# Optimization experiments

Hardware: AMD Instinct MI355X
Metric: run time of the kernel (lower is better)

The kernel has to match this reference:

```python
import jax, jax.numpy as jnp
import numpy as np

N_NODES = 100000

def setup_inputs() -> dict:
    key = jax.random.key(0)
    k1, k2, k3 = jax.random.split(key, 3)
    x = jax.random.normal(k1, (N_NODES, 64), dtype=jnp.float32)
    edge_index = jax.random.randint(k2, (2, 1250000), 0, N_NODES, dtype=jnp.int64)
    edge_weight = jax.random.uniform(k3, (1250000,), dtype=jnp.float32)
    return {"x": x, "edge_index": edge_index, "edge_weight": edge_weight}

def reference(x, edge_index, edge_weight):
    # LightGCNConv: out[dst] = sum_e edge_weight[e] * x[src_e]  (aggr='add')
    src, dst = edge_index[0], edge_index[1]
    msgs = edge_weight[:, None] * x[src]          # [E, d] gather-multiply
    out = jax.ops.segment_sum(msgs, dst, num_segments=N_NODES)  # scatter-add
    return out
```

## Files before the change

### kernel.cpp

```cpp
#include <hip/hip_runtime.h>
#include <hip/hip_bf16.h>


#define N_NODES   100000
#define N_FEAT    64

#define A_BSH     7
#define A_NPB     (1 << A_BSH)
#define A_KB      ((N_NODES + A_NPB - 1) >> A_BSH)
#define A_CAP     2048
#define A_FCHUNK  4096
#define A_OVCAP   65536
#define NBIN      ((1250000 + A_FCHUNK - 1) / A_FCHUNK)
#define NCAST     391

__global__ __launch_bounds__(1024) void k_castbin(
    const float* __restrict__ x, ushort* __restrict__ xb,
    const int* __restrict__ ei, const float* __restrict__ w,
    int* __restrict__ bcur, int2* __restrict__ stg,
    int* __restrict__ ovf, int* __restrict__ ovcnt, int E) {
    int t = threadIdx.x;
    if (blockIdx.x >= NBIN) {
        int cb = blockIdx.x - NBIN;
        #pragma unroll
        for (int k = 0; k < 4; ++k) {
            int i4 = cb * 4096 + k * 1024 + t;
            if (i4 < N_NODES * N_FEAT / 4) {
                float4 v = ((const float4*)x)[i4];
                uint4 u = *(uint4*)&v;
                ushort4 r;
                r.x = (ushort)((u.x + 0x7FFFu + ((u.x >> 16) & 1)) >> 16);
                r.y = (ushort)((u.y + 0x7FFFu + ((u.y >> 16) & 1)) >> 16);
                r.z = (ushort)((u.z + 0x7FFFu + ((u.z >> 16) & 1)) >> 16);
                r.w = (ushort)((u.w + 0x7FFFu + ((u.w >> 16) & 1)) >> 16);
                ((ushort4*)xb)[i4] = r;
            }
        }
        return;
    }
    __shared__ int h[A_KB];
    for (int b = t; b < A_KB; b += 1024) h[b] = 0;
    __syncthreads();
    int e0 = blockIdx.x * A_FCHUNK;
    int dstv[A_FCHUNK / 1024];
    int srcv[A_FCHUNK / 1024];
    float wv[A_FCHUNK / 1024];
    #pragma unroll
    for (int k = 0; k < A_FCHUNK / 1024; ++k) {
        int e = e0 + k * 1024 + t;
        bool ok = (e < E);
        dstv[k] = ok ? ei[E + e] : -1;
        srcv[k] = ok ? ei[e] : 0;
        wv[k]   = ok ? w[e] : 0.f;
        if (ok) atomicAdd(&h[dstv[k] >> A_BSH], 1);
    }
    __syncthreads();
    for (int b = t; b < A_KB; b += 1024) {
        int c = h[b];
        h[b] = c ? atomicAdd(&bcur[b], c) : 0;
    }
    __syncthreads();
    #pragma unroll
    for (int k = 0; k < A_FCHUNK / 1024; ++k) {
        if (dstv[k] >= 0) {
            int b = dstv[k] >> A_BSH;
            int loc = atomicAdd(&h[b], 1);
            if (loc < A_CAP) {
                stg[b * A_CAP + loc] =
                    make_int2(srcv[k] | ((dstv[k] & (A_NPB - 1)) << 17),
                              __float_as_int(wv[k]));
            } else {
                int oi = atomicAdd(ovcnt, 1);
                if (oi < A_OVCAP) ovf[oi] = e0 + k * 1024 + t;
            }
        }
    }
}

__global__ __launch_bounds__(1024) void k_sortgather(
    const ushort* __restrict__ xb, const int* __restrict__ bcur,
    const int2* __restrict__ stg, float* __restrict__ out) {
    __shared__ int2 buf[A_CAP];
    __shared__ int2 srt[A_CAP];
    __shared__ int  hist[A_NPB];
    __shared__ int  start[A_NPB];
    __shared__ int  cur[A_NPB];
    int b = blockIdx.x, t = threadIdx.x;
    int cnt = bcur[b];
    if (cnt > A_CAP) cnt = A_CAP;
    int base = b * A_CAP;

    if (t < A_NPB) hist[t] = 0;
    __syncthreads();
    for (int i = t; i < cnt; i += 1024) {
        int2 p = stg[base + i];
        buf[i] = p;
        atomicAdd(&hist[(p.x >> 17) & (A_NPB - 1)], 1);
    }
    __syncthreads();
    if (t < A_NPB) cur[t] = hist[t];
    __syncthreads();
    for (int off = 1; off < A_NPB; off <<= 1) {
        int v = (t < A_NPB && t >= off) ? cur[t - off] : 0;
        __syncthreads();
        if (t < A_NPB && t >= off) cur[t] += v;
        __syncthreads();
    }
    if (t < A_NPB) start[t] = (t == 0) ? 0 : cur[t - 1];
    __syncthreads();
    if (t < A_NPB) cur[t] = start[t];
    __syncthreads();
    for (int i = t; i < cnt; i += 1024) {
        int2 p = buf[i];
        int pos = atomicAdd(&cur[(p.x >> 17) & (A_NPB - 1)], 1);
        srt[pos] = p;
    }
    __syncthreads();

    int wid  = t >> 6;
    int lane = t & 63;
    int q    = lane >> 4;
    int l    = lane & 15;
    const ushort4* xb4 = (const ushort4*)xb;
    #pragma unroll
    for (int pass = 0; pass < 2; ++pass) {
        int n = pass * 64 + wid * 4 + q;
        int node = (b << A_BSH) + n;
        int j = start[n], end = start[n] + hist[n];
        float ax0 = 0.f, ay0 = 0.f, az0 = 0.f, aw0 = 0.f;
        float ax1 = 0.f, ay1 = 0.f, az1 = 0.f, aw1 = 0.f;
        for (; j + 1 < end; j += 2) {
            int2 p0 = srt[j];
            int2 p1 = srt[j + 1];
            ushort4 u0 = xb4[(size_t)(p0.x & 0x1FFFF) * 16 + l];
            ushort4 u1 = xb4[(size_t)(p1.x & 0x1FFFF) * 16 + l];
            float w0 = __int_as_float(p0.y), w1 = __int_as_float(p1.y);
            ax0 += w0 * __uint_as_float((uint)u0.x << 16);
            ay0 += w0 * __uint_as_float((uint)u0.y << 16);
            az0 += w0 * __uint_as_float((uint)u0.z << 16);
            aw0 += w0 * __uint_as_float((uint)u0.w << 16);
            ax1 += w1 * __uint_as_float((uint)u1.x << 16);
            ay1 += w1 * __uint_as_float((uint)u1.y << 16);
            az1 += w1 * __uint_as_float((uint)u1.z << 16);
            aw1 += w1 * __uint_as_float((uint)u1.w << 16);
        }
        if (j < end) {
            int2 p = srt[j];
            ushort4 u = xb4[(size_t)(p.x & 0x1FFFF) * 16 + l];
            float wv = __int_as_float(p.y);
            ax0 += wv * __uint_as_float((uint)u.x << 16);
            ay0 += wv * __uint_as_float((uint)u.y << 16);
            az0 += wv * __uint_as_float((uint)u.z << 16);
            aw0 += wv * __uint_as_float((uint)u.w << 16);
        }
        if (node < N_NODES) {
            float4 r;
            r.x = ax0 + ax1; r.y = ay0 + ay1;
            r.z = az0 + az1; r.w = aw0 + aw1;
            ((float4*)out)[(size_t)node * 16 + l] = r;
        }
    }
}

__global__ __launch_bounds__(256) void k_ovf(
    const float* __restrict__ x, const int* __restrict__ ei,
    const float* __restrict__ w, const int* __restrict__ ovf,
    const int* __restrict__ ovcnt, float* __restrict__ out, int E) {
    int n = *ovcnt;
    if (n > A_OVCAP) n = A_OVCAP;
    int wid  = blockIdx.x * 4 + (threadIdx.x >> 6);
    int lane = threadIdx.x & 63;
    for (int i = wid; i < n; i += gridDim.x * 4) {
        int e = ovf[i];
        float v = w[e] * x[(size_t)ei[e] * N_FEAT + lane];
        atomicAdd(&out[(size_t)ei[E + e] * N_FEAT + lane], v);
    }
}

#define BSH       8
#define NPB       (1 << BSH)
#define KB        ((N_NODES + NPB - 1) >> BSH)
#define FCHUNK    8192
#define SORT_CAP  4096

__global__ __launch_bounds__(256) void k_chist(
    const int* __restrict__ ei, int* __restrict__ bcur, int E) {
    __shared__ int h[KB];
    int t = threadIdx.x;
    for (int b = t; b < KB; b += 256) h[b] = 0;
    __syncthreads();
    int e0 = blockIdx.x * FCHUNK;
    #pragma unroll
    for (int k = 0; k < FCHUNK / 256; ++k) {
        int e = e0 + k * 256 + t;
        if (e < E) atomicAdd(&h[ei[E + e] >> BSH], 1);
    }
    __syncthreads();
    for (int b = t; b < KB; b += 256) if (h[b]) atomicAdd(&bcur[b], h[b]);
}

__global__ __launch_bounds__(256) void k_cscan(
    int* __restrict__ bcur, int* __restrict__ boffs) {
    __shared__ int sdata[256];
    int t = threadIdx.x;
    int i0 = 2 * t, i1 = 2 * t + 1;
    int v0 = (i0 < KB) ? bcur[i0] : 0;
    int v1 = (i1 < KB) ? bcur[i1] : 0;
    sdata[t] = v0 + v1; __syncthreads();
    for (int off = 1; off < 256; off <<= 1) {
        int v = (t >= off) ? sdata[t - off] : 0;
        __syncthreads();
        if (t >= off) sdata[t] += v;
        __syncthreads();
    }
    int run = (t == 0) ? 0 : sdata[t - 1];
    if (i0 < KB) { boffs[i0] = run; bcur[i0] = run; }
    run += v0;
    if (i1 < KB) { boffs[i1] = run; bcur[i1] = run; }
    if (t == 255) boffs[KB] = sdata[255];
}

__global__ __launch_bounds__(256) void k_cbin(
    const int* __restrict__ ei, const float* __restrict__ w,
    int* __restrict__ bcur, int2* __restrict__ stg, int E) {
    __shared__ int h[KB];
    int t = threadIdx.x;
    for (int b = t; b < KB; b += 256) h[b] = 0;
    __syncthreads();
    int e0 = blockIdx.x * FCHUNK;
    #pragma unroll
    for (int k = 0; k < FCHUNK / 256; ++k) {
        int e = e0 + k * 256 + t;
        if (e < E) atomicAdd(&h[ei[E + e] >> BSH], 1);
    }
    __syncthreads();
    for (int b = t; b < KB; b += 256) {
        int c = h[b];
        h[b] = c ? atomicAdd(&bcur[b], c) : 0;
    }
    __syncthreads();
    #pragma unroll
    for (int k = 0; k < FCHUNK / 256; ++k) {
        int e = e0 + k * 256 + t;
        if (e < E) {
            int dst = ei[E + e];
            int slot = atomicAdd(&h[dst >> BSH], 1);
            stg[slot] = make_int2(ei[e] | ((dst & (NPB - 1)) << 17),
                                  __float_as_int(w[e]));
        }
    }
}

__global__ __launch_bounds__(256) void k_csort(
    int2* __restrict__ stg, const int* __restrict__ boffs,
    int* __restrict__ offs) {
    __shared__ int2 buf[SORT_CAP];
    __shared__ int  hist[NPB];
    __shared__ int  cur[NPB];
    __shared__ int  sdata[256];
    int b = blockIdx.x, t = threadIdx.x;
    int bg = boffs[b], end = boffs[b + 1], cnt = end - bg;
    for (int n = t; n < NPB; n += 256) hist[n] = 0;
    __syncthreads();
    int nlds = cnt < SORT_CAP ? cnt : SORT_CAP;
    for (int i = t; i < nlds; i += 256) {
        int2 p = stg[bg + i];
        buf[i] = p;
        atomicAdd(&hist[(p.x >> 17) & (NPB - 1)], 1);
    }
    int2 r0{0,0}, r1{0,0}; int nr = 0;
    {
        int i0 = nlds + t, i1 = nlds + 256 + t;
        if (i0 < cnt) { r0 = stg[bg + i0]; atomicAdd(&hist[(r0.x >> 17) & (NPB - 1)], 1); nr = 1; }
        if (i1 < cnt) { r1 = stg[bg + i1]; atomicAdd(&hist[(r1.x >> 17) & (NPB - 1)], 1); nr = 2; }
    }
    __syncthreads();
    int c = hist[t];
    sdata[t] = c; __syncthreads();
    for (int off = 1; off < 256; off <<= 1) {
        int v = (t >= off) ? sdata[t - off] : 0;
        __syncthreads();
        if (t >= off) sdata[t] += v;
        __syncthreads();
    }
    int excl = (t == 0) ? 0 : sdata[t - 1];
    cur[t] = excl;
    int node = (b << BSH) + t;
    if (node < N_NODES) offs[node] = bg + excl;
    if (b == KB - 1 && t == 255) offs[N_NODES] = end;
    __syncthreads();
    for (int i = t; i < nlds; i += 256) {
        int2 p = buf[i];
        int pos = atomicAdd(&cur[(p.x >> 17) & (NPB - 1)], 1);
        stg[bg + pos] = p;
    }
    if (nr >= 1) { int pos = atomicAdd(&cur[(r0.x >> 17) & (NPB - 1)], 1); stg[bg + pos] = r0; }
    if (nr >= 2) { int pos = atomicAdd(&cur[(r1.x >> 17) & (NPB - 1)], 1); stg[bg + pos] = r1; }
}

__global__ __launch_bounds__(256) void k_gather(
    const float* __restrict__ x, const int* __restrict__ offs,
    const int2* __restrict__ stg, float* __restrict__ out) {
    int node = blockIdx.x * 4 + (threadIdx.x >> 6);
    int lane = threadIdx.x & 63;
    if (node >= N_NODES) return;
    int bg = offs[node], end = offs[node + 1];
    float a0 = 0.f, a1 = 0.f, a2 = 0.f, a3 = 0.f;
    int j = bg;
    for (; j + 3 < end; j += 4) {
        int2 p0 = stg[j];
        int2 p1 = stg[j + 1];
        int2 p2 = stg[j + 2];
        int2 p3 = stg[j + 3];
        a0 += __int_as_float(p0.y) * x[(size_t)(p0.x & 0x1FFFF) * N_FEAT + lane];
        a1 += __int_as_float(p1.y) * x[(size_t)(p1.x & 0x1FFFF) * N_FEAT + lane];
        a2 += __int_as_float(p2.y) * x[(size_t)(p2.x & 0x1FFFF) * N_FEAT + lane];
        a3 += __int_as_float(p3.y) * x[(size_t)(p3.x & 0x1FFFF) * N_FEAT + lane];
    }
    for (; j < end; ++j) {
        int2 p = stg[j];
        a0 += __int_as_float(p.y) * x[(size_t)(p.x & 0x1FFFF) * N_FEAT + lane];
    }
    out[(size_t)node * N_FEAT + lane] = (a0 + a1) + (a2 + a3);
}

__global__ __launch_bounds__(256) void gnn_scatter_kernel(
    const float* __restrict__ x, const int* __restrict__ ei,
    const float* __restrict__ w, float* __restrict__ out, int E) {
    int e = blockIdx.x * 4 + (threadIdx.x >> 6);
    int lane = threadIdx.x & 63;
    if (e >= E) return;
    float v = w[e] * x[(size_t)ei[e] * N_FEAT + lane];
    atomicAdd(&out[(size_t)ei[E + e] * N_FEAT + lane], v);
}

static inline size_t align16(size_t v) { return (v + 15) & ~(size_t)15; }

extern "C" void kernel_launch(void* const* d_in, const int* in_sizes, int n_in,
                              void* d_out, int out_size, void* d_ws, size_t ws_size,
                              hipStream_t stream) {
    const float* x   = (const float*)d_in[0];
    const int*   ei  = (const int*)d_in[1];
    const float* w   = (const float*)d_in[2];
    float*       out = (float*)d_out;
    const int E = in_sizes[2];
    char* ws = (char*)d_ws;

    size_t a_xb   = 0;
    size_t a_stg  = align16(a_xb + (size_t)N_NODES * N_FEAT * 2);
    size_t a_bcur = align16(a_stg + (size_t)A_KB * A_CAP * 8);
    size_t a_ovf  = align16(a_bcur + (size_t)(A_KB + 1) * 4);
    size_t need_a = a_ovf + (size_t)A_OVCAP * 4;

    if (ws_size >= need_a && E == 1250000) {
        ushort* xb    = (ushort*)(ws + a_xb);
        int2*   stg   = (int2*)(ws + a_stg);
        int*    bcur  = (int*)(ws + a_bcur);
        int*    ovcnt = bcur + A_KB;
        int*    ovf   = (int*)(ws + a_ovf);

        hipMemsetAsync(bcur, 0, (size_t)(A_KB + 1) * 4, stream);
        k_castbin<<<NBIN + NCAST, 1024, 0, stream>>>(
            x, xb, ei, w, bcur, stg, ovf, ovcnt, E);
        k_sortgather<<<A_KB, 1024, 0, stream>>>(xb, bcur, stg, out);
        k_ovf<<<16, 256, 0, stream>>>(x, ei, w, ovf, ovcnt, out, E);
        return;
    }

    size_t b_bcur  = 0;
    size_t b_boffs = align16(b_bcur + (size_t)KB * 4);
    size_t b_offs  = align16(b_boffs + (size_t)(KB + 1) * 4);
    size_t b_stg   = align16(b_offs + (size_t)(N_NODES + 1) * 4);
    size_t need_b  = b_stg + (size_t)E * 8;

    if (ws_size >= need_b) {
        int*  bcur  = (int*)(ws + b_bcur);
        int*  boffs = (int*)(ws + b_boffs);
        int*  offs  = (int*)(ws + b_offs);
        int2* stg   = (int2*)(ws + b_stg);
        const int nblk = (E + FCHUNK - 1) / FCHUNK;
        hipMemsetAsync(bcur, 0, (size_t)KB * 4, stream);
        k_chist<<<nblk, 256, 0, stream>>>(ei, bcur, E);
        k_cscan<<<1, 256, 0, stream>>>(bcur, boffs);
        k_cbin<<<nblk, 256, 0, stream>>>(ei, w, bcur, stg, E);
        k_csort<<<KB, 256, 0, stream>>>(stg, boffs, offs);
        k_gather<<<(N_NODES + 3) / 4, 256, 0, stream>>>(x, offs, stg, out);
        return;
    }

    hipMemsetAsync(d_out, 0, (size_t)out_size * sizeof(float), stream);
    gnn_scatter_kernel<<<(E + 3) / 4, 256, 0, stream>>>(x, ei, w, out, E);
}
```

Baseline: 135.6 us.

## Vectorize edge loads, degree-sort nodes, and gather with 8 lanes per node

The binning kernel now loads each thread's four consecutive edges with int4/float4 vector loads instead of four strided scalar loads. In the gather kernel, nodes are bitonic-sorted by in-degree within each bucket so that wavefronts process nodes of similar degree, which is meant to reduce divergence from uneven loop lengths. Each node now uses 8 lanes with 16-byte bf16 loads instead of 16 lanes with 8-byte loads, so all 128 nodes are handled in one pass. The cost is an extra shared-memory sort with many __syncthreads barriers, and more registers per thread for the wider accumulators.

```diff
diff --git a/kernel.cpp b/kernel.cpp
--- a/kernel.cpp
+++ b/kernel.cpp
@@ -42,18 +42,28 @@
     for (int b = t; b < A_KB; b += 1024) h[b] = 0;
     __syncthreads();
     int e0 = blockIdx.x * A_FCHUNK;
-    int dstv[A_FCHUNK / 1024];
-    int srcv[A_FCHUNK / 1024];
-    float wv[A_FCHUNK / 1024];
-    #pragma unroll
-    for (int k = 0; k < A_FCHUNK / 1024; ++k) {
-        int e = e0 + k * 1024 + t;
-        bool ok = (e < E);
-        dstv[k] = ok ? ei[E + e] : -1;
-        srcv[k] = ok ? ei[e] : 0;
-        wv[k]   = ok ? w[e] : 0.f;
-        if (ok) atomicAdd(&h[dstv[k] >> A_BSH], 1);
-    }
+    int ebase = e0 + t * 4;
+    int4 d4; int4 s4; float4 w4;
+    if (ebase + 3 < E) {
+        d4 = ((const int4*)(ei + E))[(e0 >> 2) + t];
+        s4 = ((const int4*)ei)[(e0 >> 2) + t];
+        w4 = ((const float4*)w)[(e0 >> 2) + t];
+    } else {
+        int* dp = (int*)&d4; int* sp = (int*)&s4; float* wp = (float*)&w4;
+        #pragma unroll
+        for (int c = 0; c < 4; ++c) {
+            int e = ebase + c;
+            dp[c] = (e < E) ? ei[E + e] : -1;
+            sp[c] = (e < E) ? ei[e] : 0;
+            wp[c] = (e < E) ? w[e] : 0.f;
+        }
+    }
+    const int* dp = (const int*)&d4;
+    const int* sp = (const int*)&s4;
+    const float* wp = (const float*)&w4;
+    #pragma unroll
+    for (int c = 0; c < 4; ++c)
+        if (dp[c] >= 0) atomicAdd(&h[dp[c] >> A_BSH], 1);
     __syncthreads();
     for (int b = t; b < A_KB; b += 1024) {
         int c = h[b];
@@ -61,17 +71,17 @@
     }
     __syncthreads();
     #pragma unroll
-    for (int k = 0; k < A_FCHUNK / 1024; ++k) {
-        if (dstv[k] >= 0) {
-            int b = dstv[k] >> A_BSH;
+    for (int c = 0; c < 4; ++c) {
+        if (dp[c] >= 0) {
+            int b = dp[c] >> A_BSH;
             int loc = atomicAdd(&h[b], 1);
             if (loc < A_CAP) {
                 stg[b * A_CAP + loc] =
-                    make_int2(srcv[k] | ((dstv[k] & (A_NPB - 1)) << 17),
-                              __float_as_int(wv[k]));
+                    make_int2(sp[c] | ((dp[c] & (A_NPB - 1)) << 17),
+                              __float_as_int(wp[c]));
             } else {
                 int oi = atomicAdd(ovcnt, 1);
-                if (oi < A_OVCAP) ovf[oi] = e0 + k * 1024 + t;
+                if (oi < A_OVCAP) ovf[oi] = ebase + c;
             }
         }
     }
@@ -85,6 +95,7 @@
     __shared__ int  hist[A_NPB];
     __shared__ int  start[A_NPB];
     __shared__ int  cur[A_NPB];
+    __shared__ int  order[A_NPB];
     int b = blockIdx.x, t = threadIdx.x;
     int cnt = bcur[b];
     if (cnt > A_CAP) cnt = A_CAP;
@@ -108,57 +119,88 @@
     }
     if (t < A_NPB) start[t] = (t == 0) ? 0 : cur[t - 1];
     __syncthreads();
-    if (t < A_NPB) cur[t] = start[t];
+    if (t < A_NPB) {
+        cur[t] = start[t];
+        order[t] = (hist[t] << A_BSH) | t;
+    }
     __syncthreads();
     for (int i = t; i < cnt; i += 1024) {
         int2 p = buf[i];
         int pos = atomicAdd(&cur[(p.x >> 17) & (A_NPB - 1)], 1);
         srt[pos] = p;
     }
+    for (int k = 2; k <= A_NPB; k <<= 1) {
+        for (int j = k >> 1; j > 0; j >>= 1) {
+            if (t < A_NPB) {
+                int ixj = t ^ j;
+                if (ixj > t) {
+                    int a = order[t], c = order[ixj];
+                    bool up = ((t & k) == 0);
+                    if (up ? (a < c) : (a > c)) { order[t] = c; order[ixj] = a; }
+                }
+            }
+            __syncthreads();
+        }
+    }
     __syncthreads();
 
     int wid  = t >> 6;
     int lane = t & 63;
-    int q    = lane >> 4;
-    int l    = lane & 15;
-    const ushort4* xb4 = (const ushort4*)xb;
-    #pragma unroll
-    for (int pass = 0; pass < 2; ++pass) {
-        int n = pass * 64 + wid * 4 + q;
-        int node = (b << A_BSH) + n;
-        int j = start[n], end = start[n] + hist[n];
-        float ax0 = 0.f, ay0 = 0.f, az0 = 0.f, aw0 = 0.f;
-        float ax1 = 0.f, ay1 = 0.f, az1 = 0.f, aw1 = 0.f;
-        for (; j + 1 < end; j += 2) {
-            int2 p0 = srt[j];
-            int2 p1 = srt[j + 1];
-            ushort4 u0 = xb4[(size_t)(p0.x & 0x1FFFF) * 16 + l];
-            ushort4 u1 = xb4[(size_t)(p1.x & 0x1FFFF) * 16 + l];
-            float w0 = __int_as_float(p0.y), w1 = __int_as_float(p1.y);
-            ax0 += w0 * __uint_as_float((uint)u0.x << 16);
-            ay0 += w0 * __uint_as_float((uint)u0.y << 16);
-            az0 += w0 * __uint_as_float((uint)u0.z << 16);
-            aw0 += w0 * __uint_as_float((uint)u0.w << 16);
-            ax1 += w1 * __uint_as_float((uint)u1.x << 16);
-            ay1 += w1 * __uint_as_float((uint)u1.y << 16);
-            az1 += w1 * __uint_as_float((uint)u1.z << 16);
-            aw1 += w1 * __uint_as_float((uint)u1.w << 16);
-        }
-        if (j < end) {
-            int2 p = srt[j];
-            ushort4 u = xb4[(size_t)(p.x & 0x1FFFF) * 16 + l];
-            float wv = __int_as_float(p.y);
-            ax0 += wv * __uint_as_float((uint)u.x << 16);
-            ay0 += wv * __uint_as_float((uint)u.y << 16);
-            az0 += wv * __uint_as_float((uint)u.z << 16);
-            aw0 += wv * __uint_as_float((uint)u.w << 16);
-        }
-        if (node < N_NODES) {
-            float4 r;
-            r.x = ax0 + ax1; r.y = ay0 + ay1;
-            r.z = az0 + az1; r.w = aw0 + aw1;
-            ((float4*)out)[(size_t)node * 16 + l] = r;
-        }
+    int s    = wid * 8 + (lane >> 3);
+    int l    = lane & 7;
+    int ord  = order[s];
+    int n    = ord & (A_NPB - 1);
+    int deg  = ord >> A_BSH;
+    int node = (b << A_BSH) + n;
+    int j = start[n], end = start[n] + deg;
+    const uint4* xb4 = (const uint4*)xb;
+    float acc0[8], acc1[8];
+    #pragma unroll
+    for (int i = 0; i < 8; ++i) { acc0[i] = 0.f; acc1[i] = 0.f; }
+    for (; j + 1 < end; j += 2) {
+        int2 p0 = srt[j];
+        int2 p1 = srt[j + 1];
+        uint4 u0 = xb4[(size_t)(p0.x & 0x1FFFF) * 8 + l];
+        uint4 u1 = xb4[(size_t)(p1.x & 0x1FFFF) * 8 + l];
+        float w0 = __int_as_float(p0.y), w1 = __int_as_float(p1.y);
+        acc0[0] += w0 * __uint_as_float(u0.x << 16);
+        acc0[1] += w0 * __uint_as_float(u0.x & 0xFFFF0000u);
+        acc0[2] += w0 * __uint_as_float(u0.y << 16);
+        acc0[3] += w0 * __uint_as_float(u0.y & 0xFFFF0000u);
+        acc0[4] += w0 * __uint_as_float(u0.z << 16);
+        acc0[5] += w0 * __uint_as_float(u0.z & 0xFFFF0000u);
+        acc0[6] += w0 * __uint_as_float(u0.w << 16);
+        acc0[7] += w0 * __uint_as_float(u0.w & 0xFFFF0000u);
+        acc1[0] += w1 * __uint_as_float(u1.x << 16);
+        acc1[1] += w1 * __uint_as_float(u1.x & 0xFFFF0000u);
+        acc1[2] += w1 * __uint_as_float(u1.y << 16);
+        acc1[3] += w1 * __uint_as_float(u1.y & 0xFFFF0000u);
+        acc1[4] += w1 * __uint_as_float(u1.z << 16);
+        acc1[5] += w1 * __uint_as_float(u1.z & 0xFFFF0000u);
+        acc1[6] += w1 * __uint_as_float(u1.w << 16);
+        acc1[7] += w1 * __uint_as_float(u1.w & 0xFFFF0000u);
+    }
+    if (j < end) {
+        int2 p = srt[j];
+        uint4 u = xb4[(size_t)(p.x & 0x1FFFF) * 8 + l];
+        float wv = __int_as_float(p.y);
+        acc0[0] += wv * __uint_as_float(u.x << 16);
+        acc0[1] += wv * __uint_as_float(u.x & 0xFFFF0000u);
+        acc0[2] += wv * __uint_as_float(u.y << 16);
+        acc0[3] += wv * __uint_as_float(u.y & 0xFFFF0000u);
+        acc0[4] += wv * __uint_as_float(u.z << 16);
+        acc0[5] += wv * __uint_as_float(u.z & 0xFFFF0000u);
+        acc0[6] += wv * __uint_as_float(u.w << 16);
+        acc0[7] += wv * __uint_as_float(u.w & 0xFFFF0000u);
+    }
+    if (node < N_NODES) {
+        float4 r0, r1;
+        r0.x = acc0[0] + acc1[0]; r0.y = acc0[1] + acc1[1];
+        r0.z = acc0[2] + acc1[2]; r0.w = acc0[3] + acc1[3];
+        r1.x = acc0[4] + acc1[4]; r1.y = acc0[5] + acc1[5];
+        r1.z = acc0[6] + acc1[6]; r1.w = acc0[7] + acc1[7];
+        ((float4*)out)[(size_t)node * 16 + l * 2]     = r0;
+        ((float4*)out)[(size_t)node * 16 + l * 2 + 1] = r1;
     }
 }
 
```

After: 145.1 us. 7.0% more time.
